# Kernel optimization log

Measured on AMD Instinct MI355X. Metric: run time of the kernel, lower is better.

## Reference

```python
import math
import jax, jax.numpy as jnp
import numpy as np

B, T, DIM = 2, 2048, 2048
HEADS, HEAD_DIM = 16, 128
KV_GROUPS = 4
N_KV = HEADS // KV_GROUPS  # 4
LATENT = 512
SEL_TOPK, SEL_HEADS, SEL_DIM = 64, 1, 64
SOFTCAP = 30.0
EPS = 1e-6


def _alibi_slopes(n):
    def pot(p):
        start = 2.0 ** (-(2.0 ** (-(math.log2(p) - 3))))
        return [start * start ** i for i in range(p)]
    if math.log2(n).is_integer():
        return pot(n)
    cp = 2 ** int(math.floor(math.log2(n)))
    s = pot(cp)
    s += _alibi_slopes(2 * cp)[0::2][: n - cp]
    return s


def _alibi_bias(h, t):
    slopes = jnp.asarray(_alibi_slopes(h), jnp.float32)
    pos = jnp.arange(t)
    dist = jnp.clip(pos[:, None] - pos[None, :], 0, None).astype(jnp.float32)  # causal clamp_min(0)
    return -slopes[:, None, None] * dist  # (H,T,T)


def _rope_emb(t, d):
    inv = 1.0 / (10000.0 ** (jnp.arange(0, d, 2, dtype=jnp.float32) / d))
    f = jnp.arange(t, dtype=jnp.float32)[:, None] * inv[None, :]
    return jnp.concatenate([f, f], axis=-1)  # (T, D)


def _apply_rotary(x, emb):
    # x: (B,T,H,D); replicates RotaryPositionalEncoding.apply_rotary exactly
    cos = jnp.cos(emb)[None, :, None, :]
    sin = jnp.sin(emb)[None, :, None, :]
    x1, x2 = x[..., 0::2], x[..., 1::2]
    c, s = cos[..., 0::2], sin[..., 0::2]
    r = jnp.stack([x1 * c - x2 * s, x1 * s + x2 * c], axis=-1)
    return r.reshape(x.shape)


def _rmsnorm(x, w):
    return x * jax.lax.rsqrt(jnp.mean(x * x, axis=-1, keepdims=True) + EPS) * w


def _forward(x, w_q, b_q, w_down, b_down, w_up, b_up, w_o, b_o, qn_w, kn_w, gate_w, gate_b):
    b, t, _ = x.shape
    # MLA projections
    q = (x @ w_q + b_q).reshape(b, t, HEADS, HEAD_DIM)
    kv = (x @ w_down + b_down) @ w_up + b_up  # (B,T,2*N_KV*D)
    k = kv[..., : N_KV * HEAD_DIM].reshape(b, t, N_KV, HEAD_DIM)
    v = kv[..., N_KV * HEAD_DIM:].reshape(b, t, N_KV, HEAD_DIM)
    # QK RMS-norm + RoPE
    q = _rmsnorm(q, qn_w)
    k = _rmsnorm(k, kn_w)
    emb = _rope_emb(t, HEAD_DIM)
    q = _apply_rotary(q, emb)
    k = _apply_rotary(k, emb)
    # GQA expand kv heads
    k = jnp.repeat(k, KV_GROUPS, axis=2)
    v = jnp.repeat(v, KV_GROUPS, axis=2)
    q = q.transpose(0, 2, 1, 3)  # (B,H,T,D)
    k = k.transpose(0, 2, 1, 3)
    v = v.transpose(0, 2, 1, 3)
    # selector top-k mask (detached)
    qs = jax.lax.stop_gradient(q[:, :SEL_HEADS, :, :SEL_DIM].astype(jnp.float32))
    ks = jax.lax.stop_gradient(k[:, :SEL_HEADS, :, :SEL_DIM].astype(jnp.float32))
    s = jnp.einsum('bhqd,bhkd->bhqk', qs, ks) / math.sqrt(SEL_DIM)
    tri = jnp.triu(jnp.ones((t, t), bool), 1)  # future positions
    s = jnp.where(tri, -jnp.inf, s)
    idx = jax.lax.top_k(s, SEL_TOPK)[1]  # (B,hs,T,K)
    sel = jnp.zeros((b, SEL_HEADS, t, t), bool)
    bi = jnp.arange(b)[:, None, None, None]
    hi = jnp.arange(SEL_HEADS)[None, :, None, None]
    ti = jnp.arange(t)[None, None, :, None]
    sel = sel.at[bi, hi, ti, idx].set(True)
    sel = sel | jnp.eye(t, dtype=bool)[None, None]  # always keep diagonal
    sel = sel & ~tri  # causal
    sel = jnp.any(sel, axis=1, keepdims=True)  # broadcast over heads (h_sel < h)
    amask = jnp.where(sel, 0.0, -jnp.inf).astype(jnp.float32)
    # attention with softcap + ALiBi
    scores = jnp.einsum('bhqd,bhkd->bhqk', q, k) / math.sqrt(HEAD_DIM)
    scores = jnp.tanh(scores / SOFTCAP) * SOFTCAP
    scores = scores + _alibi_bias(HEADS, t)[None] + amask
    attn = jax.nn.softmax(scores, axis=-1)
    y = jnp.einsum('bhqk,bhkd->bhqd', attn, v)
    # per-head dense sigmoid gating on output
    gate = jax.nn.sigmoid(jnp.einsum('bhtd,hde->bhte', y, gate_w) + gate_b[None, :, None, :])
    y = (y * gate).transpose(0, 2, 1, 3).reshape(b, t, HEADS * HEAD_DIM)
    return y @ w_o + b_o


def setup_inputs() -> dict:
    key = jax.random.key(0)
    ks = jax.random.split(key, 6)
    sd = 0.02
    return {
        'x': jax.random.normal(ks[0], (B, T, DIM), jnp.float32),
        'w_q': jax.random.normal(ks[1], (DIM, HEADS * HEAD_DIM), jnp.float32) * sd,
        'b_q': jnp.zeros((HEADS * HEAD_DIM,), jnp.float32),
        'w_down': jax.random.normal(ks[2], (DIM, LATENT), jnp.float32) * sd,
        'b_down': jnp.zeros((LATENT,), jnp.float32),
        'w_up': jax.random.normal(ks[3], (LATENT, 2 * N_KV * HEAD_DIM), jnp.float32) * sd,
        'b_up': jnp.zeros((2 * N_KV * HEAD_DIM,), jnp.float32),
        'w_o': jax.random.normal(ks[4], (HEADS * HEAD_DIM, DIM), jnp.float32) * sd,
        'b_o': jnp.zeros((DIM,), jnp.float32),
        'qn_w': jnp.ones((HEAD_DIM,), jnp.float32),
        'kn_w': jnp.ones((HEAD_DIM,), jnp.float32),
        'gate_w': jax.random.normal(ks[5], (HEADS, HEAD_DIM, HEAD_DIM), jnp.float32) * (1.0 / math.sqrt(HEAD_DIM)),
        'gate_b': jnp.zeros((HEADS, HEAD_DIM), jnp.float32),
    }


def reference(x, w_q, b_q, w_down, b_down, w_up, b_up, w_o, b_o, qn_w, kn_w, gate_w, gate_b):
    return _forward(x, w_q, b_q, w_down, b_down, w_up, b_up, w_o, b_o, qn_w, kn_w, gate_w, gate_b)
```

## Files before the change

### kernel.cpp

```cpp
#include <hip/hip_runtime.h>
#include <math.h>

#define T_SEQ 2048
#define BATCH 2
#define NHEADS 16
#define HD 128
#define NKV 4

typedef __bf16 bf16x8 __attribute__((ext_vector_type(8)));
typedef float f32x4 __attribute__((ext_vector_type(4)));

__device__ inline unsigned short bf16rne(float f) {
  unsigned u = __float_as_uint(f);
  unsigned r = (u + 0x7FFFu + ((u >> 16) & 1u)) >> 16;
  return (unsigned short)r;
}

__device__ inline float bflo(unsigned u) {
  return __uint_as_float(u << 16);
}
__device__ inline float bfhi(unsigned u) {
  return __uint_as_float(u & 0xFFFF0000u);
}

__device__ inline void gload_lds16(const void* g, void* l) {
  __builtin_amdgcn_global_load_lds(
      (__attribute__((address_space(1))) void*)const_cast<void*>(g),
      (__attribute__((address_space(3))) void*)l, 16, 0, 0);
}

#define ENC_NEGINF 0x007FFFFFu
__device__ inline unsigned enc32(float v) {
  unsigned u = __float_as_uint(v);
  return (u & 0x80000000u) ? ~u : (u | 0x80000000u);
}

__global__ void rope_table_kernel(float* __restrict__ tab) {
  int t = blockIdx.x;
  int i = threadIdx.x;
  int j = (2 * i) & 63;
  float y = (float)pow(10000.0, (double)j / 64.0);
  float invf = 1.0f / y;
  float angle = (float)t * invf;
  double a = (double)angle;
  tab[(t * 64 + i) * 2 + 0] = (float)cos(a);
  tab[(t * 64 + i) * 2 + 1] = (float)sin(a);
}

__global__ __launch_bounds__(128) void norm_rope_kernel(
    float* __restrict__ base, const float* __restrict__ w,
    const float* __restrict__ tab, int Hloc, int rowStride) {
  int blk = blockIdx.x;
  int h = blk % Hloc;
  int bt = blk / Hloc;
  int t = bt & (T_SEQ - 1);
  float* row = base + (size_t)bt * rowStride + h * HD;
  int d = threadIdx.x;
  float v = row[d];
  __shared__ float red[128];
  red[d] = v * v;
  __syncthreads();
#pragma unroll
  for (int off = 64; off > 0; off >>= 1) {
    if (d < off) red[d] += red[d + off];
    __syncthreads();
  }
  float ssum = red[0];
  __syncthreads();
  float inv = 1.0f / sqrtf(ssum / 128.0f + 1e-6f);
  float xn = v * inv * w[d];
  red[d] = xn;
  __syncthreads();
  int p = d >> 1;
  float c  = tab[(t * 64 + p) * 2 + 0];
  float sn = tab[(t * 64 + p) * 2 + 1];
  float x1 = red[p * 2], x2 = red[p * 2 + 1];
  row[d] = ((d & 1) == 0) ? (x1 * c - x2 * sn) : (x1 * sn + x2 * c);
}

__global__ __launch_bounds__(128) void kvnorm_rope_kernel(
    float* __restrict__ base, const float* __restrict__ w,
    const float* __restrict__ tab, unsigned short* __restrict__ kvb) {
  int blk = blockIdx.x;
  int h = blk % 4;
  int bt = blk / 4;
  int t = bt & (T_SEQ - 1);
  float* row = base + (size_t)bt * 1024 + h * HD;
  int d = threadIdx.x;
  float v = row[d];
  __shared__ float red[128];
  red[d] = v * v;
  __syncthreads();
#pragma unroll
  for (int off = 64; off > 0; off >>= 1) {
    if (d < off) red[d] += red[d + off];
    __syncthreads();
  }
  float ssum = red[0];
  __syncthreads();
  float inv = 1.0f / sqrtf(ssum / 128.0f + 1e-6f);
  float xn = v * inv * w[d];
  red[d] = xn;
  __syncthreads();
  int p = d >> 1;
  float c  = tab[(t * 64 + p) * 2 + 0];
  float sn = tab[(t * 64 + p) * 2 + 1];
  float x1 = red[p * 2], x2 = red[p * 2 + 1];
  float out = ((d & 1) == 0) ? (x1 * c - x2 * sn) : (x1 * sn + x2 * c);
  row[d] = out;
  size_t kb = (size_t)bt * 1024 + h * HD + d;
  kvb[kb] = bf16rne(out);
  float vv = base[(size_t)bt * 1024 + 512 + h * HD + d];
  kvb[(size_t)bt * 1024 + 512 + h * HD + d] = bf16rne(vv);
}

__global__ __launch_bounds__(256) void qnorm_rope_kernel(
    float* __restrict__ base, const float* __restrict__ w,
    const float* __restrict__ tab) {
  int row = blockIdx.x * 4 + (threadIdx.x >> 6);
  int lane = threadIdx.x & 63;
  int h = row & 15;
  int bt = row >> 4;
  int t = bt & (T_SEQ - 1);
  float* rp = base + (size_t)bt * 2048 + h * HD;
  float2 v = *(const float2*)(rp + 2 * lane);
  float ss = v.x * v.x + v.y * v.y;
#pragma unroll
  for (int off = 32; off > 0; off >>= 1) ss += __shfl_xor(ss, off);
  float inv = 1.0f / sqrtf(ss / 128.0f + 1e-6f);
  float2 wv = *(const float2*)(w + 2 * lane);
  float x1 = v.x * inv * wv.x;
  float x2 = v.y * inv * wv.y;
  float2 cs = *(const float2*)(tab + (t * 64 + lane) * 2);
  float2 o;
  o.x = x1 * cs.x - x2 * cs.y;
  o.y = x1 * cs.y + x2 * cs.x;
  *(float2*)(rp + 2 * lane) = o;
}

#define BKG 16
__global__ __launch_bounds__(256, 4) void sgemm6_kernel(
    const float* __restrict__ A,
    const float* __restrict__ W1, const float* __restrict__ bias1,
    float* __restrict__ C1, int ldw1, int ldc1, int nx1,
    const float* __restrict__ W2, const float* __restrict__ bias2,
    float* __restrict__ C2, int ldw2, int ldc2, int K) {
  __shared__ float As[BKG][68];
  int bx = blockIdx.x;
  const float* W; const float* bias; float* C; int ldw, ldc, n0;
  if (bx < nx1) {
    W = W1; bias = bias1; C = C1; ldw = ldw1; ldc = ldc1; n0 = bx * 64;
  } else {
    W = W2; bias = bias2; C = C2; ldw = ldw2; ldc = ldc2;
    n0 = (bx - nx1) * 64;
  }
  int tid = threadIdx.x;
  int tx = tid & 15;
  int ty = tid >> 4;
  int m0 = blockIdx.y * 64;
  int ar = tid >> 2, ac = (tid & 3) * 4;
  const float* Ap = A + (size_t)(m0 + ar) * K + ac;
  const float* Wb = W + n0 + tx * 4;
  float acc[4][4] = {};
  float4 av = *(const float4*)(Ap);
  for (int k0 = 0; k0 < K; k0 += BKG) {
    As[ac + 0][ar] = av.x; As[ac + 1][ar] = av.y;
    As[ac + 2][ar] = av.z; As[ac + 3][ar] = av.w;
    __syncthreads();
    float4 breg[BKG];
#pragma unroll
    for (int kk = 0; kk < BKG; kk++)
      breg[kk] = *(const float4*)(Wb + (size_t)(k0 + kk) * ldw);
    if (k0 + BKG < K) {
      av = *(const float4*)(Ap + k0 + BKG);
    }
#pragma unroll
    for (int kk = 0; kk < BKG; kk++) {
      float4 a = *(const float4*)&As[kk][ty * 4];
      float aa[4] = {a.x, a.y, a.z, a.w};
      float bb[4] = {breg[kk].x, breg[kk].y, breg[kk].z, breg[kk].w};
#pragma unroll
      for (int i = 0; i < 4; i++)
#pragma unroll
        for (int j = 0; j < 4; j++) acc[i][j] += aa[i] * bb[j];
    }
    __syncthreads();
  }
  float4 bv = *(const float4*)&bias[n0 + tx * 4];
  float bb[4] = {bv.x, bv.y, bv.z, bv.w};
#pragma unroll
  for (int i = 0; i < 4; i++) {
    float4 o;
    o.x = acc[i][0] + bb[0];
    o.y = acc[i][1] + bb[1];
    o.z = acc[i][2] + bb[2];
    o.w = acc[i][3] + bb[3];
    *(float4*)&C[(size_t)(m0 + ty * 4 + i) * ldc + n0 + tx * 4] = o;
  }
}

__global__ __launch_bounds__(256) void mfma_gemm_bt(
    const unsigned short* __restrict__ A,
    const unsigned short* __restrict__ BT,
    const float* __restrict__ bias,
    float* __restrict__ C,
    int M, int N, int K) {
  __shared__ bf16x8 lA[16][64];
  __shared__ bf16x8 lB[16][64];
  int tid = threadIdx.x;
  int w = tid >> 6, lane = tid & 63;
  int m0 = blockIdx.y * 128, n0 = blockIdx.x * 128;
  int wm = w >> 1, wn = w & 1;
  f32x4 acc[4][4] = {};
  int sr = lane & 15;
  int sk = (lane >> 4) * 8;
  const unsigned short* Abase = A + (size_t)(m0 + sr) * K + sk;
  const unsigned short* Bbase = BT + (size_t)(n0 + sr) * K + sk;

  for (int k0 = 0; k0 < K; k0 += 64) {
    __syncthreads();
#pragma unroll
    for (int c = 0; c < 4; c++) {
      int ch = w * 4 + c;
      int tt = ch >> 1, kk = ch & 1;
      gload_lds16(Abase + (size_t)(tt * 16) * K + k0 + kk * 32, &lA[ch][0]);
      gload_lds16(Bbase + (size_t)(tt * 16) * K + k0 + kk * 32, &lB[ch][0]);
    }
    __syncthreads();
#pragma unroll
    for (int kk = 0; kk < 2; kk++) {
      bf16x8 af[4], bfr[4];
#pragma unroll
      for (int t = 0; t < 4; t++) {
        af[t]  = lA[(wm * 4 + t) * 2 + kk][lane];
        bfr[t] = lB[(wn * 4 + t) * 2 + kk][lane];
      }
#pragma unroll
      for (int i = 0; i < 4; i++)
#pragma unroll
        for (int j = 0; j < 4; j++)
          acc[i][j] = __builtin_amdgcn_mfma_f32_16x16x32_bf16(
              af[i], bfr[j], acc[i][j], 0, 0, 0);
    }
  }
  int col0 = n0 + wn * 64 + (lane & 15);
  int row0 = m0 + wm * 64 + (lane >> 4) * 4;
#pragma unroll
  for (int j = 0; j < 4; j++) {
    float bv = bias[col0 + j * 16];
#pragma unroll
    for (int i = 0; i < 4; i++) {
#pragma unroll
      for (int r = 0; r < 4; r++)
        C[(size_t)(row0 + i * 16 + r) * N + col0 + j * 16] = acc[i][j][r] + bv;
    }
  }
}

__global__ __launch_bounds__(256) void convert_bf16_kernel(
    const float* __restrict__ X, unsigned short* __restrict__ Y, int n4) {
  int i = blockIdx.x * 256 + threadIdx.x;
  if (i >= n4) return;
  float4 v = ((const float4*)X)[i];
  ushort4 o;
  o.x = bf16rne(v.x); o.y = bf16rne(v.y);
  o.z = bf16rne(v.z); o.w = bf16rne(v.w);
  ((ushort4*)Y)[i] = o;
}

__global__ __launch_bounds__(256) void transpose_bf16_kernel(
    const float* __restrict__ W, unsigned short* __restrict__ WT,
    int K, int N) {
  __shared__ unsigned short t[32][33];
  int k0 = blockIdx.y * 32, n0 = blockIdx.x * 32;
  int tid = threadIdx.x;
#pragma unroll
  for (int i = 0; i < 4; i++) {
    int idx = tid + i * 256;
    int r = idx >> 5, c = idx & 31;
    t[c][r] = bf16rne(W[(size_t)(k0 + r) * N + n0 + c]);
  }
  __syncthreads();
#pragma unroll
  for (int i = 0; i < 4; i++) {
    int idx = tid + i * 256;
    int r = idx >> 5, c = idx & 31;
    WT[(size_t)(n0 + r) * K + k0 + c] = t[r][c];
  }
}

__global__ __launch_bounds__(256) void score_kernel(
    const float* __restrict__ qsel,
    const float* __restrict__ kv,
    unsigned* __restrict__ S,
    int b) {
  int tc = blockIdx.x, tr = blockIdx.y;
  if (tc > tr || tr == 0) return;
  __shared__ float qsT[64][68];
  __shared__ float ksT[64][68];
  int tid = threadIdx.x;
  int r0 = tr * 64, c0 = tc * 64;
#pragma unroll
  for (int u = 0; u < 16; u++) {
    int idx = u * 256 + tid;
    int row = idx >> 6, d = idx & 63;
    qsT[d][row] = qsel[((size_t)(b * T_SEQ + r0 + row)) * 128 + d];
  }
#pragma unroll
  for (int u = 0; u < 16; u++) {
    int idx = u * 256 + tid;
    int c = idx >> 6, d = idx & 63;
    ksT[d][c] = kv[((size_t)(b * T_SEQ + c0 + c)) * 1024 + d];
  }
  __syncthreads();
  int tx = tid & 15, ty = tid >> 4;
  float acc[4][4] = {};
  for (int d = 0; d < 64; d++) {
    float4 qv = *(const float4*)&qsT[d][ty * 4];
    float4 kx = *(const float4*)&ksT[d][tx * 4];
    float qq[4] = {qv.x, qv.y, qv.z, qv.w};
    float kk[4] = {kx.x, kx.y, kx.z, kx.w};
#pragma unroll
    for (int i = 0; i < 4; i++)
#pragma unroll
      for (int j = 0; j < 4; j++) acc[i][j] += qq[i] * kk[j];
  }
#pragma unroll
  for (int i = 0; i < 4; i++) {
    int r = r0 + ty * 4 + i;
    uint4 o;
    int c = c0 + tx * 4;
    o.x = (c + 0 <= r) ? enc32(acc[i][0] * 0.125f) : ENC_NEGINF;
    o.y = (c + 1 <= r) ? enc32(acc[i][1] * 0.125f) : ENC_NEGINF;
    o.z = (c + 2 <= r) ? enc32(acc[i][2] * 0.125f) : ENC_NEGINF;
    o.w = (c + 3 <= r) ? enc32(acc[i][3] * 0.125f) : ENC_NEGINF;
    *(uint4*)&S[(size_t)r * 2048 + c] = o;
  }
}

__global__ __launch_bounds__(256) void select_topk_kernel(
    const unsigned* __restrict__ S,
    int* __restrict__ sel_cnt, int* __restrict__ sel_idx, int b) {
  int blk = blockIdx.x;
  int r0 = blk * 4;
  int tid = threadIdx.x;

  if (r0 < 64) {
    for (int j = 0; j < 4; j++) {
      int r = r0 + j;
      int row = b * T_SEQ + r;
      if (tid == 0) sel_cnt[row] = r + 1;
      for (int c = tid; c <= r; c += 256) sel_idx[row * 66 + c] = c;
    }
    return;
  }

  int wv = tid >> 6, lane = tid & 63;
  int rr = r0 + wv;
  int row = b * T_SEQ + rr;
  int imax = rr >> 6;

  unsigned e[32];
  const unsigned* Sp = S + (size_t)rr * 2048 + lane;
#pragma unroll
  for (int i = 0; i < 32; i++) e[i] = (i <= imax) ? Sp[i * 64] : ENC_NEGINF;

  unsigned t = 0;
  for (int bit = 31; bit >= 0; --bit) {
    unsigned cand = t | (1u << bit);
    int cnt = 0;
#pragma unroll
    for (int i = 0; i < 32; i++) cnt += (e[i] >= cand) ? 1 : 0;
#pragma unroll
    for (int off = 1; off < 64; off <<= 1) cnt += __shfl_xor(cnt, off);
    if (cnt >= 64) t = cand;
  }

  unsigned long long below = (lane == 63) ? 0x7FFFFFFFFFFFFFFFull
                                          : ((1ull << lane) - 1ull);
  bool hasdiag = false;
  int base = 0;
#pragma unroll
  for (int i = 0; i < 32; i++) {
    int c = i * 64 + lane;
    bool wn = (e[i] > t);
    unsigned long long m = __ballot(wn);
    if (wn) {
      int slot = base + (int)__popcll(m & below);
      sel_idx[(size_t)row * 66 + slot] = c;
      if (c == rr) hasdiag = true;
    }
    base += (int)__popcll(m);
  }
  int g = base;
  int need = 64 - g;
  int tb = 0;
#pragma unroll
  for (int i = 0; i < 32; i++) {
    int c = i * 64 + lane;
    bool tie = (e[i] == t);
    unsigned long long m = __ballot(tie);
    int rank = tb + (int)__popcll(m & below);
    if (tie && rank < need) {
      sel_idx[(size_t)row * 66 + g + rank] = c;
      if (c == rr) hasdiag = true;
    }
    tb += (int)__popcll(m);
  }
  unsigned long long hd = __ballot(hasdiag);
  if (lane == 0) {
    sel_cnt[row] = hd ? 64 : 65;
    if (!hd) sel_idx[(size_t)row * 66 + 64] = rr;
  }
}

__global__ __launch_bounds__(256) void attn_kernel(
    const float* __restrict__ q,
    const unsigned short* __restrict__ kvb,
    const int* __restrict__ sel_cnt, const int* __restrict__ sel_idx,
    float* __restrict__ yg) {
  int blk = blockIdx.x;
  int g = blk & 3;
  int br = blk >> 2;
  int b = br >> 11;
  int r = br & (T_SEQ - 1);
  int tid = threadIdx.x;
  int lane = tid & 63, wv = tid >> 6;
  int H = g * 4 + wv;

  __shared__ unsigned kls[65 * 64];
  __shared__ float pbuf[4][68];
  __shared__ int idxs[66];

  int cnt = sel_cnt[br];
  if (tid < 66) idxs[tid] = (tid < cnt) ? sel_idx[(size_t)br * 66 + tid] : 0;
  __syncthreads();

  for (int c = tid; c < 65 * 16; c += 256) {
    int row = c >> 4, part = c & 15;
    uint4 kd = make_uint4(0u, 0u, 0u, 0u);
    if (row < cnt) {
      const unsigned short* gp = kvb
          + ((size_t)(b * T_SEQ + idxs[row])) * 1024 + g * HD + part * 8;
      kd = *(const uint4*)gp;
    }
    int slot = part ^ (row & 15);
    *(uint4*)&kls[row * 64 + slot * 4] = kd;
  }
  __syncthreads();

  double sd = 1.0;
  for (int i = 0; i <= H; i++) sd *= 0.70710678118654752440;
  float slope = (float)sd;

  const float* qrow = q + (size_t)br * 2048 + H * HD;

  int kidx = idxs[min(lane, cnt - 1)];
  int swz = lane & 15;
  const unsigned* kr = &kls[lane * 64];
  float acc = 0.f;
#pragma unroll
  for (int dd = 0; dd < 16; dd++) {
    uint4 kb = *(const uint4*)&kr[(dd ^ swz) * 4];
    float4 qa = *(const float4*)(qrow + dd * 8);
    float4 qb = *(const float4*)(qrow + dd * 8 + 4);
    acc += qa.x * bflo(kb.x) + qa.y * bfhi(kb.x);
    acc += qa.z * bflo(kb.y) + qa.w * bfhi(kb.y);
    acc += qb.x * bflo(kb.z) + qb.y * bfhi(kb.z);
    acc += qb.z * bflo(kb.w) + qb.w * bfhi(kb.w);
  }
  float sca = acc / sqrtf(128.0f);
  float tch = tanhf(sca / 30.0f) * 30.0f;
  float s = (lane < cnt) ? (tch - slope * (float)(r - kidx)) : -INFINITY;

  float stail = -INFINITY;
  if (cnt == 65) {
    int i64 = idxs[64];
    unsigned u = kls[64 * 64 + lane];
    float2 qt = *(const float2*)(qrow + 2 * lane);
    float ta = qt.x * bflo(u) + qt.y * bfhi(u);
#pragma unroll
    for (int off = 32; off > 0; off >>= 1) ta += __shfl_xor(ta, off);
    stail = tanhf(ta / sqrtf(128.0f) / 30.0f) * 30.0f
            - slope * (float)(r - i64);
  }

  float m = s;
#pragma unroll
  for (int off = 32; off > 0; off >>= 1) m = fmaxf(m, __shfl_xor(m, off));
  m = fmaxf(m, stail);
  float e = (lane < cnt) ? expf(s - m) : 0.f;
  float sum = e;
#pragma unroll
  for (int off = 32; off > 0; off >>= 1) sum += __shfl_xor(sum, off);
  float et = (cnt == 65) ? expf(stail - m) : 0.f;
  sum += et;
  pbuf[wv][lane] = e / sum;
  if (lane == 0) pbuf[wv][64] = et / sum;
  if (lane >= 1 && lane <= 3) pbuf[wv][64 + lane] = 0.f;

  const unsigned short* vbase = kvb + (size_t)b * T_SEQ * 1024 + 512 + g * HD;
  float y0 = 0.f, y1 = 0.f;
  int jmax = (cnt + 3) >> 2;
  for (int j4 = 0; j4 < jmax; j4++) {
    float4 p4 = *(const float4*)&pbuf[wv][j4 * 4];
    float pp[4] = {p4.x, p4.y, p4.z, p4.w};
#pragma unroll
    for (int t = 0; t < 4; t++) {
      int ij = idxs[min(j4 * 4 + t, cnt - 1)];
      unsigned u = *(const unsigned*)(vbase + (size_t)ij * 1024 + 2 * lane);
      y0 += pp[t] * bflo(u);
      y1 += pp[t] * bfhi(u);
    }
  }
  float2 o;
  o.x = y0;
  o.y = y1;
  *(float2*)(yg + (size_t)br * 2048 + H * HD + 2 * lane) = o;
}

__global__ __launch_bounds__(256) void gate_kernel(
    const float* __restrict__ yg, unsigned short* __restrict__ ygb,
    const float* __restrict__ gw, const float* __restrict__ gb) {
  int blk = blockIdx.x;
  int h = blk & 15;
  int bt0 = (blk >> 4) * 16;
  int tid = threadIdx.x;
  __shared__ float ys[16][128];
  for (int i = tid; i < 16 * 128; i += 256) {
    int rr = i >> 7, d = i & 127;
    ys[rr][d] = yg[(size_t)(bt0 + rr) * 2048 + h * HD + d];
  }
  __syncthreads();
  int e = tid & 127;
  int rblk = tid >> 7;
  const float* gwp = gw + (size_t)h * 16384 + e;
  float acc[8] = {};
  for (int d = 0; d < 128; d++) {
    float wval = gwp[(size_t)d * 128];
#pragma unroll
    for (int k = 0; k < 8; k++) acc[k] += ys[rblk * 8 + k][d] * wval;
  }
  float bb = gb[h * 128 + e];
#pragma unroll
  for (int k = 0; k < 8; k++) {
    int rr = rblk * 8 + k;
    float gate = 1.f / (1.f + expf(-(acc[k] + bb)));
    ygb[(size_t)(bt0 + rr) * 2048 + h * HD + e] = bf16rne(ys[rr][e] * gate);
  }
}

extern "C" void kernel_launch(void* const* d_in, const int* in_sizes, int n_in,
                              void* d_out, int out_size, void* d_ws, size_t ws_size,
                              hipStream_t stream) {
  const float* x      = (const float*)d_in[0];
  const float* w_q    = (const float*)d_in[1];
  const float* b_q    = (const float*)d_in[2];
  const float* w_down = (const float*)d_in[3];
  const float* b_down = (const float*)d_in[4];
  const float* w_up   = (const float*)d_in[5];
  const float* b_up   = (const float*)d_in[6];
  const float* w_o    = (const float*)d_in[7];
  const float* b_o    = (const float*)d_in[8];
  const float* qn_w   = (const float*)d_in[9];
  const float* kn_w   = (const float*)d_in[10];
  const float* gate_w = (const float*)d_in[11];
  const float* gate_b = (const float*)d_in[12];

  float* ws    = (float*)d_ws;
  float* kvbuf = ws;
  float* yg    = ws + 4194304;
  float* dlat  = yg;
  float* tab   = ws + 12582912;
  int*   cnt   = (int*)(ws + 12845056);
  int*   sidx  = cnt + 4096;
  float* qsel  = ws + 13120000;
  unsigned short* xb  = (unsigned short*)(ws + 13906432);
  unsigned short* dlatb = xb;
  unsigned short* ygb = xb;
  unsigned* Sbuf = (unsigned*)xb;
  unsigned short* wT  = xb + 8388608;
  unsigned short* wupT = wT;
  unsigned short* kvb  = wT;

  float* qbuf = (float*)d_out;
  const int BT = BATCH * T_SEQ;

  rope_table_kernel<<<T_SEQ, 64, 0, stream>>>(tab);
  convert_bf16_kernel<<<8192, 256, 0, stream>>>(x, xb, 2097152);
  transpose_bf16_kernel<<<dim3(64, 64), 256, 0, stream>>>(w_q, wT, 2048, 2048);
  mfma_gemm_bt<<<dim3(16, 32), 256, 0, stream>>>(xb, wT, b_q, qbuf,
                                                 BT, 2048, 2048);
  sgemm6_kernel<<<dim3(10, 64), 256, 0, stream>>>(
      x, w_q, b_q, qsel, 2048, 128, 2,
      w_down, b_down, dlat, 512, 512, 2048);
  convert_bf16_kernel<<<2048, 256, 0, stream>>>(dlat, dlatb, 524288);
  transpose_bf16_kernel<<<dim3(32, 16), 256, 0, stream>>>(w_up, wupT,
                                                          512, 1024);
  mfma_gemm_bt<<<dim3(8, 32), 256, 0, stream>>>(dlatb, wupT, b_up, kvbuf,
                                                BT, 1024, 512);
  sgemm6_kernel<<<dim3(2, 64), 256, 0, stream>>>(
      dlat, w_up, b_up, kvbuf, 1024, 1024, 2,
      w_up, b_up, kvbuf, 1024, 1024, 512);
  qnorm_rope_kernel<<<BT * 4, 256, 0, stream>>>(qbuf, qn_w, tab);
  norm_rope_kernel<<<BT, 128, 0, stream>>>(qsel, qn_w, tab, 1, 128);
  kvnorm_rope_kernel<<<BT * 4, 128, 0, stream>>>(kvbuf, kn_w, tab, kvb);
  for (int b = 0; b < BATCH; b++) {
    score_kernel<<<dim3(32, 32), 256, 0, stream>>>(qsel, kvbuf, Sbuf, b);
    select_topk_kernel<<<512, 256, 0, stream>>>(Sbuf, cnt, sidx, b);
  }
  attn_kernel<<<BT * 4, 256, 0, stream>>>(qbuf, kvb, cnt, sidx, yg);
  gate_kernel<<<(BT / 16) * 16, 256, 0, stream>>>(yg, ygb, gate_w, gate_b);
  transpose_bf16_kernel<<<dim3(64, 64), 256, 0, stream>>>(w_o, wT, 2048, 2048);
  mfma_gemm_bt<<<dim3(16, 32), 256, 0, stream>>>(ygb, wT, b_o, (float*)d_out,
                                                 BT, 2048, 2048);
}
```

Before: 824.5 us.

## Batch score/top-k launches across batch and stage W tile in shared memory

The score and top-k selection kernels now cover both batches in a single launch each, using blockIdx.z or the high bits of blockIdx.x, with a full per-batch score buffer placed in the yg workspace region. This removes the per-batch serialization and gives each launch more blocks. The fp32 side GEMM now stages the weight tile in shared memory with a register prefetch, instead of having each thread load 16 float4 rows straight from global memory. The change relies on the yg region being free until attention writes it; dlat aliases it but is consumed earlier.

```diff
diff --git a/kernel.cpp b/kernel.cpp
--- a/kernel.cpp
+++ b/kernel.cpp
@@ -139,13 +139,14 @@
 }
 
 #define BKG 16
-__global__ __launch_bounds__(256, 4) void sgemm6_kernel(
+__global__ __launch_bounds__(256) void sgemm3_kernel(
     const float* __restrict__ A,
     const float* __restrict__ W1, const float* __restrict__ bias1,
     float* __restrict__ C1, int ldw1, int ldc1, int nx1,
     const float* __restrict__ W2, const float* __restrict__ bias2,
     float* __restrict__ C2, int ldw2, int ldc2, int K) {
   __shared__ float As[BKG][68];
+  __shared__ float Bs[BKG][68];
   int bx = blockIdx.x;
   const float* W; const float* bias; float* C; int ldw, ldc, n0;
   if (bx < nx1) {
@@ -159,26 +160,27 @@
   int ty = tid >> 4;
   int m0 = blockIdx.y * 64;
   int ar = tid >> 2, ac = (tid & 3) * 4;
+  int brr = tid >> 4, bc = (tid & 15) * 4;
   const float* Ap = A + (size_t)(m0 + ar) * K + ac;
-  const float* Wb = W + n0 + tx * 4;
+  const float* Wp = W + (size_t)brr * ldw + n0 + bc;
   float acc[4][4] = {};
   float4 av = *(const float4*)(Ap);
+  float4 wv = *(const float4*)(Wp);
   for (int k0 = 0; k0 < K; k0 += BKG) {
     As[ac + 0][ar] = av.x; As[ac + 1][ar] = av.y;
     As[ac + 2][ar] = av.z; As[ac + 3][ar] = av.w;
+    *(float4*)&Bs[brr][bc] = wv;
     __syncthreads();
-    float4 breg[BKG];
-#pragma unroll
-    for (int kk = 0; kk < BKG; kk++)
-      breg[kk] = *(const float4*)(Wb + (size_t)(k0 + kk) * ldw);
     if (k0 + BKG < K) {
       av = *(const float4*)(Ap + k0 + BKG);
+      wv = *(const float4*)(Wp + (size_t)(k0 + BKG) * ldw);
     }
 #pragma unroll
     for (int kk = 0; kk < BKG; kk++) {
       float4 a = *(const float4*)&As[kk][ty * 4];
+      float4 b = *(const float4*)&Bs[kk][tx * 4];
       float aa[4] = {a.x, a.y, a.z, a.w};
-      float bb[4] = {breg[kk].x, breg[kk].y, breg[kk].z, breg[kk].w};
+      float bb[4] = {b.x, b.y, b.z, b.w};
 #pragma unroll
       for (int i = 0; i < 4; i++)
 #pragma unroll
@@ -292,10 +294,11 @@
 __global__ __launch_bounds__(256) void score_kernel(
     const float* __restrict__ qsel,
     const float* __restrict__ kv,
-    unsigned* __restrict__ S,
-    int b) {
+    unsigned* __restrict__ S) {
   int tc = blockIdx.x, tr = blockIdx.y;
+  int b = blockIdx.z;
   if (tc > tr || tr == 0) return;
+  unsigned* Sb = S + (size_t)b * T_SEQ * T_SEQ;
   __shared__ float qsT[64][68];
   __shared__ float ksT[64][68];
   int tid = threadIdx.x;
@@ -334,14 +337,16 @@
     o.y = (c + 1 <= r) ? enc32(acc[i][1] * 0.125f) : ENC_NEGINF;
     o.z = (c + 2 <= r) ? enc32(acc[i][2] * 0.125f) : ENC_NEGINF;
     o.w = (c + 3 <= r) ? enc32(acc[i][3] * 0.125f) : ENC_NEGINF;
-    *(uint4*)&S[(size_t)r * 2048 + c] = o;
+    *(uint4*)&Sb[(size_t)r * 2048 + c] = o;
   }
 }
 
 __global__ __launch_bounds__(256) void select_topk_kernel(
     const unsigned* __restrict__ S,
-    int* __restrict__ sel_cnt, int* __restrict__ sel_idx, int b) {
-  int blk = blockIdx.x;
+    int* __restrict__ sel_cnt, int* __restrict__ sel_idx) {
+  int b = blockIdx.x >> 9;
+  int blk = blockIdx.x & 511;
+  const unsigned* Sb = S + (size_t)b * T_SEQ * T_SEQ;
   int r0 = blk * 4;
   int tid = threadIdx.x;
 
@@ -361,7 +366,7 @@
   int imax = rr >> 6;
 
   unsigned e[32];
-  const unsigned* Sp = S + (size_t)rr * 2048 + lane;
+  const unsigned* Sp = Sb + (size_t)rr * 2048 + lane;
 #pragma unroll
   for (int i = 0; i < 32; i++) e[i] = (i <= imax) ? Sp[i * 64] : ENC_NEGINF;
 
@@ -571,6 +576,7 @@
   float* kvbuf = ws;
   float* yg    = ws + 4194304;
   float* dlat  = yg;
+  unsigned* Sfull = (unsigned*)yg;
   float* tab   = ws + 12582912;
   int*   cnt   = (int*)(ws + 12845056);
   int*   sidx  = cnt + 4096;
@@ -578,7 +584,6 @@
   unsigned short* xb  = (unsigned short*)(ws + 13906432);
   unsigned short* dlatb = xb;
   unsigned short* ygb = xb;
-  unsigned* Sbuf = (unsigned*)xb;
   unsigned short* wT  = xb + 8388608;
   unsigned short* wupT = wT;
   unsigned short* kvb  = wT;
@@ -591,7 +596,7 @@
   transpose_bf16_kernel<<<dim3(64, 64), 256, 0, stream>>>(w_q, wT, 2048, 2048);
   mfma_gemm_bt<<<dim3(16, 32), 256, 0, stream>>>(xb, wT, b_q, qbuf,
                                                  BT, 2048, 2048);
-  sgemm6_kernel<<<dim3(10, 64), 256, 0, stream>>>(
+  sgemm3_kernel<<<dim3(10, 64), 256, 0, stream>>>(
       x, w_q, b_q, qsel, 2048, 128, 2,
       w_down, b_down, dlat, 512, 512, 2048);
   convert_bf16_kernel<<<2048, 256, 0, stream>>>(dlat, dlatb, 524288);
@@ -599,16 +604,14 @@
                                                           512, 1024);
   mfma_gemm_bt<<<dim3(8, 32), 256, 0, stream>>>(dlatb, wupT, b_up, kvbuf,
                                                 BT, 1024, 512);
-  sgemm6_kernel<<<dim3(2, 64), 256, 0, stream>>>(
+  sgemm3_kernel<<<dim3(2, 64), 256, 0, stream>>>(
       dlat, w_up, b_up, kvbuf, 1024, 1024, 2,
       w_up, b_up, kvbuf, 1024, 1024, 512);
   qnorm_rope_kernel<<<BT * 4, 256, 0, stream>>>(qbuf, qn_w, tab);
   norm_rope_kernel<<<BT, 128, 0, stream>>>(qsel, qn_w, tab, 1, 128);
   kvnorm_rope_kernel<<<BT * 4, 128, 0, stream>>>(kvbuf, kn_w, tab, kvb);
-  for (int b = 0; b < BATCH; b++) {
-    score_kernel<<<dim3(32, 32), 256, 0, stream>>>(qsel, kvbuf, Sbuf, b);
-    select_topk_kernel<<<512, 256, 0, stream>>>(Sbuf, cnt, sidx, b);
-  }
+  score_kernel<<<dim3(32, 32, 2), 256, 0, stream>>>(qsel, kvbuf, Sfull);
+  select_topk_kernel<<<1024, 256, 0, stream>>>(Sfull, cnt, sidx);
   attn_kernel<<<BT * 4, 256, 0, stream>>>(qbuf, kvb, cnt, sidx, yg);
   gate_kernel<<<(BT / 16) * 16, 256, 0, stream>>>(yg, ygb, gate_w, gate_b);
   transpose_bf16_kernel<<<dim3(64, 64), 256, 0, stream>>>(w_o, wT, 2048, 2048);
```

New measurement: 723.7 us. 1.14x faster.
